# Kernel optimization log

Measured on AMD Instinct MI355X. Metric: run time of the kernel, lower is better.

## Reference

```python
import jax, jax.numpy as jnp
import numpy as np

V = 32000; D = 1024; L = 2; H = 16; KVH = 4; HD = D // H; E = 8; FF = 2048; K = 2
B = 2; S = 1024; WINDOW = 4096; THETA = 10000.0; EPS = 1e-6


def setup_inputs() -> dict:
    key = jax.random.key(0)
    ks = jax.random.split(key, 12)
    std = 0.02
    return {
        'tokens': jax.random.randint(ks[0], (B, S), 0, V),
        'tok_emb': jax.random.normal(ks[1], (V, D), jnp.float32),  # nn.Embedding default N(0,1)
        'norm1_w': jnp.ones((L, D), jnp.float32),
        'norm2_w': jnp.ones((L, D), jnp.float32),
        'wq': jax.random.normal(ks[2], (L, D, D), jnp.float32) * std,
        'wk': jax.random.normal(ks[3], (L, KVH * HD, D), jnp.float32) * std,
        'wv': jax.random.normal(ks[4], (L, KVH * HD, D), jnp.float32) * std,
        'wo': jax.random.normal(ks[5], (L, D, D), jnp.float32) * std,
        'router_w': jax.random.normal(ks[6], (L, E, D), jnp.float32) * (std / np.sqrt(D)),
        'w1': jax.random.normal(ks[7], (L, E, FF, D), jnp.float32) * std,
        'w2': jax.random.normal(ks[8], (L, E, FF, D), jnp.float32) * std,
        'w3': jax.random.normal(ks[9], (L, E, D, FF), jnp.float32) * std,
        'normf_w': jnp.ones((D,), jnp.float32),
        'head_w': jax.random.normal(ks[10], (V, D), jnp.float32) * std,
    }


def rmsnorm(x, w):
    # F.normalize(x, dim=-1, eps) * w * sqrt(d)
    n = jnp.linalg.norm(x, axis=-1, keepdims=True)
    return x / jnp.maximum(n, EPS) * w * np.float32(np.sqrt(x.shape[-1]))


def rope(x, cos, sin):
    # x: (b, s, h, hd); pairs are interleaved (even, odd) per view_as_complex
    x2 = x.reshape(x.shape[:-1] + (-1, 2))
    x0, x1 = x2[..., 0], x2[..., 1]
    o0 = x0 * cos - x1 * sin
    o1 = x0 * sin + x1 * cos
    return jnp.stack([o0, o1], axis=-1).reshape(x.shape)


def attention(x, wq, wk, wv, wo, cos, sin):
    b, s, _ = x.shape
    q = (x @ wq.T).reshape(b, s, H, HD)
    k = (x @ wk.T).reshape(b, s, KVH, HD)
    v = (x @ wv.T).reshape(b, s, KVH, HD)
    q = rope(q, cos, sin)
    k = rope(k, cos, sin)
    g = H // KVH
    k = jnp.repeat(k, g, axis=2)
    v = jnp.repeat(v, g, axis=2)
    scores = jnp.einsum('bqhd,bkhd->bhqk', q, k) / np.float32(np.sqrt(HD))
    i = jnp.arange(s)[:, None]; j = jnp.arange(s)[None, :]
    allow = (j <= i) & (i - j < WINDOW)  # causal + sliding window
    scores = jnp.where(allow, scores, -jnp.inf)
    attn = jax.nn.softmax(scores, axis=-1)
    out = jnp.einsum('bhqk,bkhd->bqhd', attn, v).reshape(b, s, D)
    return out @ wo.T


def moe(x, router_w, w1, w2, w3):
    b, s, d = x.shape
    logits = jnp.einsum('bsd,ed->bse', x, router_w)
    probs = jax.nn.softmax(logits, axis=-1)
    _, idx = jax.lax.top_k(probs, K)                      # (b, s, K)
    mask = jax.nn.one_hot(idx, E, dtype=x.dtype).sum(-2)  # (b, s, E) binary
    xt = x.reshape(-1, d)           # (T, d)
    mt = mask.reshape(-1, E)        # (T, E)
    # Dense masked dispatch: every expert computed on all tokens, combine masks to zero
    u = jnp.einsum('td,efd->etf', xt, w1)
    g = jax.nn.silu(u) * jnp.einsum('td,efd->etf', xt, w2)
    y = jnp.einsum('etf,edf->etd', g, w3)
    out = jnp.einsum('etd,te->td', y, mt).reshape(b, s, d)  # unweighted combine (per source)
    # aux losses
    z_loss = jnp.mean(jax.scipy.special.logsumexp(logits, axis=-1)) ** 2
    load = probs.sum(axis=0)  # (s, E), matching probs.sum(dim=0) in source
    load_loss = (jnp.std(load, ddof=1) / jnp.mean(load)) ** 2
    aux = 0.001 * z_loss + 0.001 * load_loss
    return out, aux


def _rope_tables(dtype):
    freqs = 1.0 / (THETA ** (np.arange(0, HD, 2, dtype=np.float32) / HD))
    ang = np.arange(S, dtype=np.float32)[:, None] * freqs[None, :]
    cos = jnp.asarray(np.cos(ang), dtype)[None, :, None, :]
    sin = jnp.asarray(np.sin(ang), dtype)[None, :, None, :]
    return cos, sin


def reference(tokens, tok_emb, norm1_w, norm2_w, wq, wk, wv, wo, router_w, w1, w2, w3, normf_w, head_w):
    x = tok_emb[tokens]  # (B, S, D)
    cos, sin = _rope_tables(x.dtype)
    attn_scale = np.float32(1.0 / np.sqrt(2.0 * L))
    aux_total = jnp.zeros((), x.dtype)
    for l in range(L):
        x = x + attn_scale * attention(rmsnorm(x, norm1_w[l]), wq[l], wk[l], wv[l], wo[l], cos, sin)
        mo, aux = moe(rmsnorm(x, norm2_w[l]), router_w[l], w1[l], w2[l], w3[l])
        x = x + mo
        aux_total = aux_total + aux
    logits = rmsnorm(x, normf_w) @ head_w.T
    return logits, aux_total
```

## Files before the change

### kernel.cpp

```cpp
#include <hip/hip_runtime.h>
#include <math.h>

#define DEV __device__ __forceinline__

using v8s = __attribute__((ext_vector_type(8))) short;
using v4f = __attribute__((ext_vector_type(4))) float;

DEV short f2bf(float f) {
    unsigned u = __float_as_uint(f);
    unsigned r = (u + 0x7fffu + ((u >> 16) & 1u)) >> 16;
    return (short)(unsigned short)r;
}
DEV float bf2f(short s) {
    return __uint_as_float(((unsigned)(unsigned short)s) << 16);
}

DEV void gload16(const short* g, short* l) {
    __builtin_amdgcn_global_load_lds((const __attribute__((address_space(1))) void*)g,
                                     (__attribute__((address_space(3))) void*)l,
                                     16, 0, 0);
}

DEV float block_sum256(float v, float* red) {
    __syncthreads();
#pragma unroll
    for (int o = 32; o >= 1; o >>= 1) v += __shfl_down(v, o, 64);
    if ((threadIdx.x & 63) == 0) red[threadIdx.x >> 6] = v;
    __syncthreads();
    return red[0] + red[1] + red[2] + red[3];
}
DEV float block_max256(float v, float* red) {
    __syncthreads();
#pragma unroll
    for (int o = 32; o >= 1; o >>= 1) v = fmaxf(v, __shfl_down(v, o, 64));
    if ((threadIdx.x & 63) == 0) red[threadIdx.x >> 6] = v;
    __syncthreads();
    return fmaxf(fmaxf(red[0], red[1]), fmaxf(red[2], red[3]));
}


__global__ __launch_bounds__(256) void conv_tile(const float* __restrict__ src,
                                                 short* __restrict__ hi, short* __restrict__ lo,
                                                 long nGroups, int Kg, long chunkRows, long chunkPanelStride) {
    const long panelElems = 128L * Kg * 8;
    for (long idx = (long)blockIdx.x * 256 + threadIdx.x; idx < nGroups; idx += (long)gridDim.x * 256) {
        long rrow = idx / Kg; int g = (int)(idx - rrow * Kg);
        int kblk = g >> 2, kg = g & 3;
        long c = rrow / chunkRows; int ri = (int)(rrow - c * chunkRows);
        long panel = c * chunkPanelStride + (ri >> 7);
        int row = ri & 127;
        long dst = panel * panelElems + (long)kblk * 4096 + kg * 1024 + row * 8;
        const float4 f0 = ((const float4*)src)[idx * 2];
        const float4 f1 = ((const float4*)src)[idx * 2 + 1];
        short h0 = f2bf(f0.x), h1 = f2bf(f0.y), h2 = f2bf(f0.z), h3 = f2bf(f0.w);
        short h4 = f2bf(f1.x), h5 = f2bf(f1.y), h6 = f2bf(f1.z), h7 = f2bf(f1.w);
        *(ushort4*)(hi + dst)     = make_ushort4((unsigned short)h0, (unsigned short)h1,
                                                 (unsigned short)h2, (unsigned short)h3);
        *(ushort4*)(hi + dst + 4) = make_ushort4((unsigned short)h4, (unsigned short)h5,
                                                 (unsigned short)h6, (unsigned short)h7);
        if (lo) {
            short l0 = f2bf(f0.x - bf2f(h0)), l1 = f2bf(f0.y - bf2f(h1));
            short l2 = f2bf(f0.z - bf2f(h2)), l3 = f2bf(f0.w - bf2f(h3));
            short l4 = f2bf(f1.x - bf2f(h4)), l5 = f2bf(f1.y - bf2f(h5));
            short l6 = f2bf(f1.z - bf2f(h6)), l7 = f2bf(f1.w - bf2f(h7));
            *(ushort4*)(lo + dst)     = make_ushort4((unsigned short)l0, (unsigned short)l1,
                                                     (unsigned short)l2, (unsigned short)l3);
            *(ushort4*)(lo + dst + 4) = make_ushort4((unsigned short)l4, (unsigned short)l5,
                                                     (unsigned short)l6, (unsigned short)l7);
        }
    }
}

struct GemmP {
    const short* Ah; const short* Al;
    const short* Bh; const short* Bl;
    float* C; short* Ch; short* Cl;
    const int* cnt; const int* prefix; const int* ltok; const int* lrow;
    long strideAz, strideBz, strideCz;
    int M, N, K, lda, ldc;
    float alpha;
    int outMode;
    int gqaB;
    int attnC;
    int grouped;
    int causalSkip;
    int causalK;
    int ntiles, S, G;
};

template<bool SPLIT>
__global__ __launch_bounds__(256) void gemm_bt(GemmP p) {
    const int lid = blockIdx.x;
    const int xcd = lid & 7, sI = lid >> 3;
    const int gi = xcd + 8 * (sI / p.S);
    if (gi >= p.G) return;
    const int mt = sI % p.S;
    const int nt = gi % p.ntiles;
    const int z  = gi / p.ntiles;
    if (p.causalSkip && nt > mt) return;

    const int tid = threadIdx.x;

    int Mz = p.M;
    const int* ltokz = nullptr; const int* lrowz = nullptr; int pz = 0;
    if (p.grouped) {
        Mz = p.cnt[z]; pz = p.prefix[z];
        ltokz = p.ltok + z * 2048; lrowz = p.lrow + z * 2048;
    }
    if (mt * 128 >= Mz) return;

    long aOff = (long)z * p.strideAz;
    long bOff, cOff;
    if (p.gqaB) { int b = z >> 4, h = z & 15; bOff = (long)(b * 4 + (h >> 2)) * p.strideBz; }
    else bOff = (long)z * p.strideBz;
    if (p.attnC) { int b = z >> 4, h = z & 15; cOff = (long)b * 1048576 + h * 64; }
    else cOff = (long)z * p.strideCz;

    extern __shared__ char smem[];
    short* Ahs = (short*)smem;
    short* Bhs = Ahs + 4096;
    short* Als = Bhs + 4096;
    short* Bls = Als + 4096;

    const int lane = tid & 63, w = tid >> 6;
    const int lr = lane & 15, lg = lane >> 4;
    const int wr = w >> 1, wc = w & 1;

    v4f acc[4][4];
#pragma unroll
    for (int i = 0; i < 4; ++i)
#pragma unroll
        for (int j = 0; j < 4; ++j) { acc[i][j][0] = 0.f; acc[i][j][1] = 0.f; acc[i][j][2] = 0.f; acc[i][j][3] = 0.f; }

    const int r = tid & 127;
    const int kgA = tid >> 7;
    int am = mt * 128 + r; if (am >= Mz) am = Mz - 1;
    long arowoff;
    if (p.grouped == 1)      arowoff = (long)ltokz[am] * p.lda;
    else if (p.grouped == 2) arowoff = (long)(pz + am) * p.lda;
    else                     arowoff = aOff + (long)am * p.lda;
    const short* aH = p.Ah + arowoff + kgA * 16;
    const short* aL = SPLIT ? p.Al + arowoff + kgA * 16 : nullptr;
    short* sA0 = Ahs + (kgA * 256 + r) * 8;
    short* sA1 = sA0 + 1024;
    short* sA0l = Als + (kgA * 256 + r) * 8;
    short* sA1l = sA0l + 1024;

    const short* bks  = p.Bh + bOff + (long)nt * 128 * p.K + (long)w * 1024 + lane * 8;
    const short* bksL = SPLIT ? p.Bl + bOff + (long)nt * 128 * p.K + (long)w * 1024 + lane * 8 : nullptr;
    short* dB  = Bhs + w * 1024;
    short* dBl = Bls + w * 1024;

    const int kEnd = p.causalK ? min(p.K, (mt + 1) * 128) : p.K;

    for (int k0 = 0; k0 < kEnd; k0 += 32) {
        const long kb = (long)k0 * 128;
        uint4 a0 = *(const uint4*)(aH + k0);
        uint4 a1 = *(const uint4*)(aH + k0 + 8);
        uint4 a0l, a1l;
        if (SPLIT) { a0l = *(const uint4*)(aL + k0); a1l = *(const uint4*)(aL + k0 + 8); }
        __syncthreads();
        gload16(bks + kb,       dB);
        gload16(bks + kb + 512, dB + 512);
        if (SPLIT) {
            gload16(bksL + kb,       dBl);
            gload16(bksL + kb + 512, dBl + 512);
        }
        *(uint4*)sA0 = a0; *(uint4*)sA1 = a1;
        if (SPLIT) { *(uint4*)sA0l = a0l; *(uint4*)sA1l = a1l; }
        __syncthreads();
        const int abase = lg * 1024 + (wr * 64 + lr) * 8;
        const int bbase = lg * 1024 + (wc * 64 + lr) * 8;
        v8s ah[4], bh[4];
#pragma unroll
        for (int i = 0; i < 4; ++i) {
            ah[i] = *(const v8s*)(Ahs + abase + i * 128);
            bh[i] = *(const v8s*)(Bhs + bbase + i * 128);
        }
        if constexpr (SPLIT) {
            v8s al[4], bl[4];
#pragma unroll
            for (int i = 0; i < 4; ++i) {
                al[i] = *(const v8s*)(Als + abase + i * 128);
                bl[i] = *(const v8s*)(Bls + bbase + i * 128);
            }
#pragma unroll
            for (int mi = 0; mi < 4; ++mi)
#pragma unroll
                for (int nj = 0; nj < 4; ++nj) {
                    acc[mi][nj] = __builtin_amdgcn_mfma_f32_16x16x32_bf16(ah[mi], bh[nj], acc[mi][nj], 0, 0, 0);
                    acc[mi][nj] = __builtin_amdgcn_mfma_f32_16x16x32_bf16(al[mi], bh[nj], acc[mi][nj], 0, 0, 0);
                    acc[mi][nj] = __builtin_amdgcn_mfma_f32_16x16x32_bf16(ah[mi], bl[nj], acc[mi][nj], 0, 0, 0);
                }
        } else {
#pragma unroll
            for (int mi = 0; mi < 4; ++mi)
#pragma unroll
                for (int nj = 0; nj < 4; ++nj)
                    acc[mi][nj] = __builtin_amdgcn_mfma_f32_16x16x32_bf16(ah[mi], bh[nj], acc[mi][nj], 0, 0, 0);
        }
    }

#pragma unroll
    for (int mi = 0; mi < 4; ++mi) {
        const int mrow = mt * 128 + wr * 64 + mi * 16 + lg * 4;
#pragma unroll
        for (int nj = 0; nj < 4; ++nj) {
            const int ncol = nt * 128 + wc * 64 + nj * 16 + lr;
            if (ncol < p.N) {
#pragma unroll
                for (int rr = 0; rr < 4; ++rr) {
                    const int m = mrow + rr;
                    if (m < Mz) {
                        float v = acc[mi][nj][rr] * p.alpha;
                        long crow;
                        if (p.grouped == 1) crow = pz + m;
                        else if (p.grouped == 2) crow = lrowz[m];
                        else crow = m;
                        long co = cOff + crow * (long)p.ldc + ncol;
                        if (p.outMode == 0) p.C[co] = v;
                        else if (p.outMode == 1) p.C[co] += v;
                        else {
                            short hi = f2bf(v);
                            p.Ch[co] = hi;
                            p.Cl[co] = f2bf(v - bf2f(hi));
                        }
                    }
                }
            }
        }
    }
}

__global__ __launch_bounds__(256) void embed_kernel(const int* toks, const float* emb, float* X) {
    const int t = blockIdx.x;
    const int tok = toks[t];
    const float4* s = (const float4*)(emb + (size_t)tok * 1024);
    float4* d = (float4*)(X + (size_t)t * 1024);
    d[threadIdx.x] = s[threadIdx.x];
}

__global__ __launch_bounds__(256) void rmsnorm_split(const float* X, const float* w, short* oh, short* ol) {
    __shared__ float red[4];
    const long t = blockIdx.x;
    const float* r = X + t * 1024;
    float ss = 0.f;
    for (int j = threadIdx.x; j < 1024; j += 256) { float f = r[j]; ss += f * f; }
    ss = block_sum256(ss, red);
    const float sc = 32.f / fmaxf(sqrtf(ss), 1e-6f);
    for (int j = threadIdx.x; j < 1024; j += 256) {
        float f = r[j] * sc * w[j];
        short hi = f2bf(f);
        oh[t * 1024 + j] = hi;
        ol[t * 1024 + j] = f2bf(f - bf2f(hi));
    }
}

struct RopeF { float f[32]; };

__global__ __launch_bounds__(256) void rope_q_kernel(const float* QKV, short* OH, short* OL, RopeF rf) {
    const int idx = blockIdx.x * 256 + threadIdx.x;
    const int pp = idx & 31, h = (idx >> 5) & 15, s = (idx >> 9) & 1023, b = idx >> 19;
    const float* src = QKV + ((size_t)(b * 1024 + s)) * 1536 + h * 64 + 2 * pp;
    const float x0 = src[0], x1 = src[1];
    const float ang = (float)s * rf.f[pp];
    float sn, cs; sincosf(ang, &sn, &cs);
    const float o0 = x0 * cs - x1 * sn, o1 = x0 * sn + x1 * cs;
    const size_t o = ((size_t)((b * 16 + h) * 1024 + s)) * 64 + 2 * pp;
    short h0 = f2bf(o0); OH[o] = h0; OL[o] = f2bf(o0 - bf2f(h0));
    short h1 = f2bf(o1); OH[o + 1] = h1; OL[o + 1] = f2bf(o1 - bf2f(h1));
}

__global__ __launch_bounds__(256) void rope_k_kernel(const float* QKV, short* KH, short* KL, RopeF rf) {
    const int idx = blockIdx.x * 256 + threadIdx.x;
    const int pp = idx & 31, kv = (idx >> 5) & 3, s = (idx >> 7) & 1023, b = idx >> 17;
    const float* src = QKV + ((size_t)(b * 1024 + s)) * 1536 + 1024 + kv * 64 + 2 * pp;
    const float x0 = src[0], x1 = src[1];
    const float ang = (float)s * rf.f[pp];
    float sn, cs; sincosf(ang, &sn, &cs);
    const float o0 = x0 * cs - x1 * sn, o1 = x0 * sn + x1 * cs;
    const int z = b * 4 + kv, d = 2 * pp;
    const long off = (long)z * 65536 + (long)(s >> 7) * 8192
                   + ((long)(d >> 5) << 12) + ((long)((d >> 3) & 3) << 10)
                   + ((long)(s & 127) << 3) + (d & 7);
    short h0 = f2bf(o0); KH[off] = h0; KL[off] = f2bf(o0 - bf2f(h0));
    short h1 = f2bf(o1); KH[off + 1] = h1; KL[off + 1] = f2bf(o1 - bf2f(h1));
}

__global__ __launch_bounds__(256) void transpose_v_kernel(const float* QKV, short* VH, short* VL) {
    const int idx = blockIdx.x * 256 + threadIdx.x;
    const int d = idx & 63, kv = (idx >> 6) & 3, s = (idx >> 8) & 1023, b = idx >> 18;
    const float f = QKV[((size_t)(b * 1024 + s)) * 1536 + 1280 + kv * 64 + d];
    const int z = b * 4 + kv;
    const long off = (long)z * 131072 + ((long)(s >> 5) << 12) + ((long)((s >> 3) & 3) << 10)
                   + ((long)d << 3) + (s & 7);
    short hi = f2bf(f);
    VH[off] = hi; VL[off] = f2bf(f - bf2f(hi));
    VH[off + 512] = 0; VL[off + 512] = 0;
}

__global__ __launch_bounds__(256) void attn_softmax(float* SC) {
    const long row = blockIdx.x;
    const int i = (int)(row & 1023);
    float* r = SC + row * 1024;
    __shared__ float buf[1024];
    __shared__ float red[4];
    const int n = i + 1;
    for (int j = threadIdx.x; j < 1024; j += 256) buf[j] = r[j];
    __syncthreads();
    float m = -INFINITY;
    for (int j = threadIdx.x; j < n; j += 256) m = fmaxf(m, buf[j]);
    m = block_max256(m, red);
    float s = 0.f;
    for (int j = threadIdx.x; j < n; j += 256) { float e = expf(buf[j] - m); buf[j] = e; s += e; }
    s = block_sum256(s, red);
    const float inv = 1.f / s;
    short* rh = (short*)r;
    short* rl = rh + 1024;
    __syncthreads();
    for (int j = threadIdx.x; j < 1024; j += 256) {
        float pv = (j < n) ? buf[j] * inv : 0.f;
        short hi = f2bf(pv);
        rh[j] = hi;
        rl[j] = f2bf(pv - bf2f(hi));
    }
}

__global__ __launch_bounds__(256) void router_kernel(const float* X, const float* wn, const float* rw,
                                                     float* probs, float* lse, int* cnt, int* ltok, int* lrow) {
    __shared__ float xs[1024];
    __shared__ float red[4];
    __shared__ float lg[8];
    const int t = blockIdx.x;
    const float* r = X + (size_t)t * 1024;
    for (int j = threadIdx.x; j < 1024; j += 256) xs[j] = r[j];
    __syncthreads();
    float ss = 0.f;
    for (int j = threadIdx.x; j < 1024; j += 256) ss += xs[j] * xs[j];
    ss = block_sum256(ss, red);
    const float sc = 32.f / fmaxf(sqrtf(ss), 1e-6f);
    float acc[8] = {0, 0, 0, 0, 0, 0, 0, 0};
    for (int j = threadIdx.x; j < 1024; j += 256) {
        const float xv = xs[j] * wn[j];
#pragma unroll
        for (int e = 0; e < 8; ++e) acc[e] += xv * rw[e * 1024 + j];
    }
#pragma unroll
    for (int e = 0; e < 8; ++e) {
        float s = block_sum256(acc[e], red);
        if (threadIdx.x == 0) lg[e] = s * sc;
    }
    __syncthreads();
    if (threadIdx.x == 0) {
        float m = lg[0];
        for (int e = 1; e < 8; ++e) m = fmaxf(m, lg[e]);
        float ex[8], se = 0.f;
        for (int e = 0; e < 8; ++e) { ex[e] = expf(lg[e] - m); se += ex[e]; }
        const float inv = 1.f / se;
        float pr[8];
        for (int e = 0; e < 8; ++e) { pr[e] = ex[e] * inv; probs[(size_t)t * 8 + e] = pr[e]; }
        lse[t] = m + logf(se);
        int i1 = 0;
        for (int e = 1; e < 8; ++e) if (pr[e] > pr[i1]) i1 = e;
        int i2 = (i1 == 0) ? 1 : 0;
        for (int e = 0; e < 8; ++e) if (e != i1 && pr[e] > pr[i2]) i2 = e;
        int s1 = atomicAdd(&cnt[i1], 1); ltok[i1 * 2048 + s1] = t; lrow[i1 * 2048 + s1] = 2 * t;
        int s2 = atomicAdd(&cnt[i2], 1); ltok[i2 * 2048 + s2] = t; lrow[i2 * 2048 + s2] = 2 * t + 1;
    }
}

__global__ void prefix_kernel(const int* cnt, int* pref) {
    if (threadIdx.x == 0 && blockIdx.x == 0) {
        int a = 0;
        for (int e = 0; e < 8; ++e) { pref[e] = a; a += cnt[e]; }
    }
}

__global__ __launch_bounds__(256) void silu_mul(const float* U, short* HH, short* HL) {
    const long i4 = (long)blockIdx.x * 256 + threadIdx.x;
    const int f4 = (int)(i4 & 511), row = (int)(i4 >> 9);
    const float4 u = *(const float4*)(U + ((long)row << 12) + (f4 << 2));
    const float4 g = *(const float4*)(U + ((long)row << 12) + 2048 + (f4 << 2));
    float h[4];
    h[0] = (u.x / (1.f + expf(-u.x))) * g.x;
    h[1] = (u.y / (1.f + expf(-u.y))) * g.y;
    h[2] = (u.z / (1.f + expf(-u.z))) * g.z;
    h[3] = (u.w / (1.f + expf(-u.w))) * g.w;
    const long o = (long)row * 2048 + (f4 << 2);
    short h0 = f2bf(h[0]), h1 = f2bf(h[1]), h2 = f2bf(h[2]), h3 = f2bf(h[3]);
    *(ushort4*)(HH + o) = make_ushort4((unsigned short)h0, (unsigned short)h1,
                                       (unsigned short)h2, (unsigned short)h3);
    short l0 = f2bf(h[0] - bf2f(h0)), l1 = f2bf(h[1] - bf2f(h1));
    short l2 = f2bf(h[2] - bf2f(h2)), l3 = f2bf(h[3] - bf2f(h3));
    *(ushort4*)(HL + o) = make_ushort4((unsigned short)l0, (unsigned short)l1,
                                       (unsigned short)l2, (unsigned short)l3);
}

__global__ __launch_bounds__(256) void combine_kernel(float* X, const float* Y) {
    const int i4 = blockIdx.x * 256 + threadIdx.x;
    const int t = i4 >> 8, d4 = i4 & 255;
    float4 x = ((float4*)X)[i4];
    const float4 a = ((const float4*)Y)[(size_t)(2 * t) * 256 + d4];
    const float4 b = ((const float4*)Y)[(size_t)(2 * t + 1) * 256 + d4];
    x.x += a.x + b.x; x.y += a.y + b.y; x.z += a.z + b.z; x.w += a.w + b.w;
    ((float4*)X)[i4] = x;
}

__global__ __launch_bounds__(256) void aux_kernel(const float* probs, const float* lse, float* auxb, int layer) {
    __shared__ float red[4];
    float sl = 0.f;
    for (int t = threadIdx.x; t < 2048; t += 256) sl += lse[t];
    sl = block_sum256(sl, red);
    float s1 = 0.f, s2 = 0.f;
    for (int i = threadIdx.x; i < 8192; i += 256) {
        const float l = probs[i] + probs[8192 + i];
        s1 += l; s2 += l * l;
    }
    s1 = block_sum256(s1, red);
    s2 = block_sum256(s2, red);
    if (threadIdx.x == 0) {
        const float ml = sl / 2048.f;
        const float mean = s1 / 8192.f;
        const float var = fmaxf((s2 - s1 * s1 / 8192.f) / 8191.f, 0.f);
        auxb[layer] = 0.001f * (ml * ml + var / (mean * mean));
    }
}

__global__ void finalize_aux(const float* auxb, float* out) {
    if (threadIdx.x == 0 && blockIdx.x == 0)
        out[(size_t)2 * 1024 * 32000] = auxb[0] + auxb[1];
}

static void run_gemm(hipStream_t s, bool split, GemmP& p, int ntiles, int mtiles, int zdim) {
    p.ntiles = ntiles; p.S = mtiles;
    p.G = ntiles * zdim;
    int Gp = (p.G + 7) & ~7;
    long nb = (long)Gp * mtiles;
    dim3 g((unsigned)nb, 1, 1), b(256);
    if (split) gemm_bt<true><<<g, b, 32768, s>>>(p);
    else       gemm_bt<false><<<g, b, 16384, s>>>(p);
}

static void run_tile(hipStream_t s, const float* src, short* hi, short* lo,
                     long rows, int K, long chunkRows, long chunkPanelStride) {
    long groups = rows * (K / 8);
    long nb = (groups + 255) / 256; if (nb > 2048) nb = 2048;
    conv_tile<<<(unsigned)nb, 256, 0, s>>>(src, hi, lo, groups, K / 8, chunkRows, chunkPanelStride);
}

extern "C" void kernel_launch(void* const* d_in, const int* in_sizes, int n_in,
                              void* d_out, int out_size, void* d_ws, size_t ws_size,
                              hipStream_t stream) {
    (void)in_sizes; (void)n_in; (void)out_size; (void)ws_size;
    const int*   tokens = (const int*)d_in[0];
    const float* tok_emb = (const float*)d_in[1];
    const float* norm1 = (const float*)d_in[2];
    const float* norm2 = (const float*)d_in[3];
    const float* wq = (const float*)d_in[4];
    const float* wk = (const float*)d_in[5];
    const float* wv = (const float*)d_in[6];
    const float* wo = (const float*)d_in[7];
    const float* rw = (const float*)d_in[8];
    const float* w1 = (const float*)d_in[9];
    const float* w2 = (const float*)d_in[10];
    const float* w3 = (const float*)d_in[11];
    const float* normf = (const float*)d_in[12];
    const float* headw = (const float*)d_in[13];
    float* out = (float*)d_out;

    char* w = (char*)d_ws;
    const size_t MB = 1024ull * 1024ull;
    float* X    = (float*)(w + 0);
    short* XNH  = (short*)(w + 8 * MB);
    short* XNL  = (short*)(w + 12 * MB);
    short* QRH  = (short*)(w + 16 * MB);
    short* QRL  = (short*)(w + 20 * MB);
    short* AOH  = QRH;
    short* AOL  = QRL;
    short* KRH  = (short*)(w + 24 * MB);
    short* KRL  = (short*)(w + 25 * MB);
    short* VTH  = (short*)(w + 26 * MB);
    short* VTL  = (short*)(w + 28 * MB);
    float* QKV  = (float*)(w + 32 * MB);
    float* SC   = (float*)(w + 32 * MB);
    float* U    = (float*)(w + 32 * MB);
    short* HH   = (short*)(w + 96 * MB);
    short* HL   = (short*)(w + 112 * MB);
    float* Y    = (float*)(w + 128 * MB);
    float* PROBS= (float*)(w + 160 * MB);
    float* LSE  = (float*)(w + 160 * MB + 65536);
    int*   CNT  = (int*)  (w + 160 * MB + 73728);
    int*   PREF = (int*)  (w + 160 * MB + 73856);
    int*   LTOK = (int*)  (w + 160 * MB + 74240);
    int*   LROW = (int*)  (w + 160 * MB + 74240 + 65536);
    float* AUXB = (float*)(w + 160 * MB + 74240 + 131072);
    short* WQKVH = (short*)(w + 162 * MB);
    short* WQKVL = (short*)(w + 168 * MB);
    short* WOH   = (short*)(w + 174 * MB);
    short* WOL   = (short*)(w + 178 * MB);
    short* W12H  = (short*)(w + 182 * MB);
    short* W12L  = (short*)(w + 246 * MB);
    short* W3H   = (short*)(w + 310 * MB);
    short* W3L   = (short*)(w + 342 * MB);
    short* HDH   = (short*)(w + 374 * MB);

    RopeF rf;
    for (int i = 0; i < 32; ++i) {
        float t = (float)pow(10000.0, (double)(2 * i) / 64.0);
        rf.f[i] = 1.0f / t;
    }

    for (int l = 0; l < 2; ++l) {
        long qo = (long)l * 1572864;
        run_tile(stream, wq + (long)l * 1048576, WQKVH + qo,           WQKVL + qo,           1024, 1024, 1024, 8);
        run_tile(stream, wk + (long)l * 262144,  WQKVH + qo + 1048576, WQKVL + qo + 1048576, 256, 1024, 256, 2);
        run_tile(stream, wv + (long)l * 262144,  WQKVH + qo + 1310720, WQKVL + qo + 1310720, 256, 1024, 256, 2);
    }
    run_tile(stream, wo, WOH, WOL, 2048, 1024, 2048, 16);
    run_tile(stream, headw, HDH, nullptr, 32000, 1024, 32000, 250);

    embed_kernel<<<2048, 256, 0, stream>>>(tokens, tok_emb, X);

    for (int l = 0; l < 2; ++l) {
        const bool msp = (l == 0);
        run_tile(stream, w1 + (long)l * 16777216, W12H,           msp ? W12L : nullptr,           16384, 1024, 2048, 32);
        run_tile(stream, w2 + (long)l * 16777216, W12H + 2097152, msp ? W12L + 2097152 : nullptr, 16384, 1024, 2048, 32);
        run_tile(stream, w3 + (long)l * 16777216, W3H,            msp ? W3L : nullptr,            8192, 2048, 8192, 64);

        rmsnorm_split<<<2048, 256, 0, stream>>>(X, norm1 + l * 1024, XNH, XNL);

        { GemmP p = {}; p.Ah = XNH; p.Al = XNL; p.Bh = WQKVH + (long)l * 1572864; p.Bl = WQKVL + (long)l * 1572864;
          p.C = QKV; p.M = 2048; p.N = 1536; p.K = 1024; p.lda = 1024; p.ldc = 1536; p.alpha = 1.f;
          run_gemm(stream, true, p, 12, 16, 1); }

        rope_q_kernel<<<4096, 256, 0, stream>>>(QKV, QRH, QRL, rf);
        rope_k_kernel<<<1024, 256, 0, stream>>>(QKV, KRH, KRL, rf);
        transpose_v_kernel<<<2048, 256, 0, stream>>>(QKV, VTH, VTL);

        { GemmP p = {}; p.Ah = QRH; p.Al = QRL; p.Bh = KRH; p.Bl = KRL; p.C = SC;
          p.M = 1024; p.N = 1024; p.K = 64; p.lda = 64; p.ldc = 1024;
          p.strideAz = 65536; p.strideBz = 65536; p.strideCz = 1048576;
          p.alpha = 0.125f; p.gqaB = 1; p.causalSkip = 1;
          run_gemm(stream, true, p, 8, 8, 32); }

        attn_softmax<<<32768, 256, 0, stream>>>(SC);

        { GemmP p = {}; p.Ah = (short*)SC; p.Al = (short*)SC + 1024; p.Bh = VTH; p.Bl = VTL; p.Ch = AOH; p.Cl = AOL;
          p.M = 1024; p.N = 64; p.K = 1024; p.lda = 2048; p.ldc = 1024;
          p.strideAz = 2097152; p.strideBz = 131072;
          p.alpha = 1.f; p.gqaB = 1; p.attnC = 1; p.causalK = 1; p.outMode = 2;
          run_gemm(stream, true, p, 1, 8, 32); }

        { GemmP p = {}; p.Ah = AOH; p.Al = AOL; p.Bh = WOH + (long)l * 1048576; p.Bl = WOL + (long)l * 1048576; p.C = X;
          p.M = 2048; p.N = 1024; p.K = 1024; p.lda = 1024; p.ldc = 1024;
          p.alpha = 0.5f; p.outMode = 1;
          run_gemm(stream, true, p, 8, 16, 1); }

        rmsnorm_split<<<2048, 256, 0, stream>>>(X, norm2 + l * 1024, XNH, XNL);
        hipMemsetAsync(CNT, 0, 8 * sizeof(int), stream);
        router_kernel<<<2048, 256, 0, stream>>>(X, norm2 + l * 1024, rw + (size_t)l * 8 * 1024,
                                                PROBS, LSE, CNT, LTOK, LROW);
        prefix_kernel<<<1, 64, 0, stream>>>(CNT, PREF);

        { GemmP p = {}; p.Ah = XNH; p.Al = XNL; p.Bh = W12H; p.Bl = W12L; p.C = U;
          p.M = 2048; p.N = 4096; p.K = 1024; p.lda = 1024; p.ldc = 4096;
          p.strideBz = 4194304; p.alpha = 1.f; p.grouped = 1;
          p.cnt = CNT; p.prefix = PREF; p.ltok = LTOK; p.lrow = LROW;
          run_gemm(stream, msp, p, 32, 16, 8); }
        silu_mul<<<8192, 256, 0, stream>>>(U, HH, HL);
        { GemmP p = {}; p.Ah = HH; p.Al = HL; p.Bh = W3H; p.Bl = W3L; p.C = Y;
          p.M = 2048; p.N = 1024; p.K = 2048; p.lda = 2048; p.ldc = 1024;
          p.strideBz = 2097152; p.alpha = 1.f; p.grouped = 2;
          p.cnt = CNT; p.prefix = PREF; p.ltok = LTOK; p.lrow = LROW;
          run_gemm(stream, msp, p, 8, 16, 8); }
        combine_kernel<<<2048, 256, 0, stream>>>(X, Y);
        aux_kernel<<<1, 256, 0, stream>>>(PROBS, LSE, AUXB, l);
    }

    rmsnorm_split<<<2048, 256, 0, stream>>>(X, normf, XNH, XNL);
    { GemmP p = {}; p.Ah = XNH; p.Bh = HDH; p.C = out;
      p.M = 2048; p.N = 32000; p.K = 1024; p.lda = 1024; p.ldc = 32000; p.alpha = 1.f;
      run_gemm(stream, false, p, 250, 16, 1); }
    finalize_aux<<<1, 1, 0, stream>>>(AUXB, out);
}
```

Before: 2.310 ms.

## Pre-tile GEMM A operands so A loads use direct global-to-LDS copies

Producers of GEMM A operands (rmsnorm, rope_q, silu_mul, the attention output epilogue) now write the same 128-row panel layout used for B. The GEMM can then stream A through global_load_lds instead of register loads followed by LDS stores. MoE tokens are gathered into per-expert padded panels by a new gather kernel, and the head weight conversion is moved later so it can share buffer space with the W12 low half. The cost is an extra gather pass, padded expert segments, and scattered per-element stores in the rope and attention epilogues.

Result: slower. 2.375 ms (+2.8%).

```diff
diff --git a/kernel.cpp b/kernel.cpp
--- a/kernel.cpp
+++ b/kernel.cpp
@@ -36,6 +36,10 @@
     if ((threadIdx.x & 63) == 0) red[threadIdx.x >> 6] = v;
     __syncthreads();
     return fmaxf(fmaxf(red[0], red[1]), fmaxf(red[2], red[3]));
+}
+
+DEV long tile_goff(int row, int g) {
+    return ((long)(g >> 2) << 12) + ((long)(g & 3) << 10) + ((long)(row & 127) << 3);
 }
 
 
@@ -45,11 +49,9 @@
     const long panelElems = 128L * Kg * 8;
     for (long idx = (long)blockIdx.x * 256 + threadIdx.x; idx < nGroups; idx += (long)gridDim.x * 256) {
         long rrow = idx / Kg; int g = (int)(idx - rrow * Kg);
-        int kblk = g >> 2, kg = g & 3;
         long c = rrow / chunkRows; int ri = (int)(rrow - c * chunkRows);
         long panel = c * chunkPanelStride + (ri >> 7);
-        int row = ri & 127;
-        long dst = panel * panelElems + (long)kblk * 4096 + kg * 1024 + row * 8;
+        long dst = panel * panelElems + ((long)(g >> 2) << 12) + ((long)(g & 3) << 10) + ((long)(ri & 127) << 3);
         const float4 f0 = ((const float4*)src)[idx * 2];
         const float4 f1 = ((const float4*)src)[idx * 2 + 1];
         short h0 = f2bf(f0.x), h1 = f2bf(f0.y), h2 = f2bf(f0.z), h3 = f2bf(f0.w);
@@ -75,20 +77,21 @@
     const short* Ah; const short* Al;
     const short* Bh; const short* Bl;
     float* C; short* Ch; short* Cl;
-    const int* cnt; const int* prefix; const int* ltok; const int* lrow;
-    long strideAz, strideBz, strideCz;
+    const int* cnt; const int* ppd; const int* lrow;
+    long aPanelsZ;
+    long strideAz;
+    long strideBz, strideCz;
     int M, N, K, lda, ldc;
     float alpha;
     int outMode;
     int gqaB;
-    int attnC;
     int grouped;
     int causalSkip;
     int causalK;
     int ntiles, S, G;
 };
 
-template<bool SPLIT>
+template<bool SPLIT, bool AREG>
 __global__ __launch_bounds__(256) void gemm_bt(GemmP p) {
     const int lid = blockIdx.x;
     const int xcd = lid & 7, sI = lid >> 3;
@@ -101,20 +104,12 @@
 
     const int tid = threadIdx.x;
 
-    int Mz = p.M;
-    const int* ltokz = nullptr; const int* lrowz = nullptr; int pz = 0;
-    if (p.grouped) {
-        Mz = p.cnt[z]; pz = p.prefix[z];
-        ltokz = p.ltok + z * 2048; lrowz = p.lrow + z * 2048;
-    }
+    int Mz = p.grouped ? p.cnt[z] : p.M;
     if (mt * 128 >= Mz) return;
 
-    long aOff = (long)z * p.strideAz;
-    long bOff, cOff;
+    long bOff;
     if (p.gqaB) { int b = z >> 4, h = z & 15; bOff = (long)(b * 4 + (h >> 2)) * p.strideBz; }
     else bOff = (long)z * p.strideBz;
-    if (p.attnC) { int b = z >> 4, h = z & 15; cOff = (long)b * 1048576 + h * 64; }
-    else cOff = (long)z * p.strideCz;
 
     extern __shared__ char smem[];
     short* Ahs = (short*)smem;
@@ -132,33 +127,42 @@
 #pragma unroll
         for (int j = 0; j < 4; ++j) { acc[i][j][0] = 0.f; acc[i][j][1] = 0.f; acc[i][j][2] = 0.f; acc[i][j][3] = 0.f; }
 
-    const int r = tid & 127;
-    const int kgA = tid >> 7;
-    int am = mt * 128 + r; if (am >= Mz) am = Mz - 1;
-    long arowoff;
-    if (p.grouped == 1)      arowoff = (long)ltokz[am] * p.lda;
-    else if (p.grouped == 2) arowoff = (long)(pz + am) * p.lda;
-    else                     arowoff = aOff + (long)am * p.lda;
-    const short* aH = p.Ah + arowoff + kgA * 16;
-    const short* aL = SPLIT ? p.Al + arowoff + kgA * 16 : nullptr;
-    short* sA0 = Ahs + (kgA * 256 + r) * 8;
-    short* sA1 = sA0 + 1024;
-    short* sA0l = Als + (kgA * 256 + r) * 8;
-    short* sA1l = sA0l + 1024;
-
     const short* bks  = p.Bh + bOff + (long)nt * 128 * p.K + (long)w * 1024 + lane * 8;
     const short* bksL = SPLIT ? p.Bl + bOff + (long)nt * 128 * p.K + (long)w * 1024 + lane * 8 : nullptr;
     short* dB  = Bhs + w * 1024;
     short* dBl = Bls + w * 1024;
 
+    const short *aks = nullptr, *aksL = nullptr;
+    short *dA = nullptr, *dAl = nullptr;
+    const short *aH = nullptr, *aL = nullptr;
+    short *sA0 = nullptr, *sA1 = nullptr, *sA0l = nullptr, *sA1l = nullptr;
+    if constexpr (AREG) {
+        const int r = tid & 127;
+        const int kgA = tid >> 7;
+        int am = mt * 128 + r; if (am >= Mz) am = Mz - 1;
+        long arowoff = (long)z * p.strideAz + (long)am * p.lda;
+        aH = p.Ah + arowoff + kgA * 16;
+        aL = SPLIT ? p.Al + arowoff + kgA * 16 : nullptr;
+        sA0 = Ahs + (kgA * 256 + r) * 8; sA1 = sA0 + 1024;
+        sA0l = Als + (kgA * 256 + r) * 8; sA1l = sA0l + 1024;
+    } else {
+        long aPanel = (p.grouped ? (long)(p.ppd[z] >> 7) : (long)z * p.aPanelsZ) + mt;
+        aks  = p.Ah + aPanel * 128L * p.K + (long)w * 1024 + lane * 8;
+        aksL = SPLIT ? p.Al + aPanel * 128L * p.K + (long)w * 1024 + lane * 8 : nullptr;
+        dA  = Ahs + w * 1024;
+        dAl = Als + w * 1024;
+    }
+
     const int kEnd = p.causalK ? min(p.K, (mt + 1) * 128) : p.K;
 
     for (int k0 = 0; k0 < kEnd; k0 += 32) {
         const long kb = (long)k0 * 128;
-        uint4 a0 = *(const uint4*)(aH + k0);
-        uint4 a1 = *(const uint4*)(aH + k0 + 8);
-        uint4 a0l, a1l;
-        if (SPLIT) { a0l = *(const uint4*)(aL + k0); a1l = *(const uint4*)(aL + k0 + 8); }
+        uint4 a0, a1, a0l, a1l;
+        if constexpr (AREG) {
+            a0 = *(const uint4*)(aH + k0);
+            a1 = *(const uint4*)(aH + k0 + 8);
+            if (SPLIT) { a0l = *(const uint4*)(aL + k0); a1l = *(const uint4*)(aL + k0 + 8); }
+        }
         __syncthreads();
         gload16(bks + kb,       dB);
         gload16(bks + kb + 512, dB + 512);
@@ -166,8 +170,17 @@
             gload16(bksL + kb,       dBl);
             gload16(bksL + kb + 512, dBl + 512);
         }
-        *(uint4*)sA0 = a0; *(uint4*)sA1 = a1;
-        if (SPLIT) { *(uint4*)sA0l = a0l; *(uint4*)sA1l = a1l; }
+        if constexpr (AREG) {
+            *(uint4*)sA0 = a0; *(uint4*)sA1 = a1;
+            if (SPLIT) { *(uint4*)sA0l = a0l; *(uint4*)sA1l = a1l; }
+        } else {
+            gload16(aks + kb,       dA);
+            gload16(aks + kb + 512, dA + 512);
+            if (SPLIT) {
+                gload16(aksL + kb,       dAl);
+                gload16(aksL + kb + 512, dAl + 512);
+            }
+        }
         __syncthreads();
         const int abase = lg * 1024 + (wr * 64 + lr) * 8;
         const int bbase = lg * 1024 + (wc * 64 + lr) * 8;
@@ -213,17 +226,22 @@
                     const int m = mrow + rr;
                     if (m < Mz) {
                         float v = acc[mi][nj][rr] * p.alpha;
-                        long crow;
-                        if (p.grouped == 1) crow = pz + m;
-                        else if (p.grouped == 2) crow = lrowz[m];
-                        else crow = m;
-                        long co = cOff + crow * (long)p.ldc + ncol;
-                        if (p.outMode == 0) p.C[co] = v;
-                        else if (p.outMode == 1) p.C[co] += v;
-                        else {
+                        if (p.outMode == 3) {
+                            int b = z >> 4, h = z & 15;
+                            int grow = b * 1024 + m, col = h * 64 + ncol;
+                            long dst = ((long)(grow >> 7)) * 131072 + ((long)(col >> 5) << 12)
+                                     + ((long)((col >> 3) & 3) << 10) + ((long)(grow & 127) << 3) + (col & 7);
                             short hi = f2bf(v);
-                            p.Ch[co] = hi;
-                            p.Cl[co] = f2bf(v - bf2f(hi));
+                            p.Ch[dst] = hi;
+                            p.Cl[dst] = f2bf(v - bf2f(hi));
+                        } else {
+                            long crow;
+                            if (p.grouped == 1)      crow = p.ppd[z] + m;
+                            else if (p.grouped == 2) crow = p.lrow[z * 2048 + m];
+                            else                     crow = m;
+                            long co = (long)z * p.strideCz + crow * (long)p.ldc + ncol;
+                            if (p.outMode == 0) p.C[co] = v;
+                            else                p.C[co] += v;
                         }
                     }
                 }
@@ -248,11 +266,19 @@
     for (int j = threadIdx.x; j < 1024; j += 256) { float f = r[j]; ss += f * f; }
     ss = block_sum256(ss, red);
     const float sc = 32.f / fmaxf(sqrtf(ss), 1e-6f);
-    for (int j = threadIdx.x; j < 1024; j += 256) {
-        float f = r[j] * sc * w[j];
-        short hi = f2bf(f);
-        oh[t * 1024 + j] = hi;
-        ol[t * 1024 + j] = f2bf(f - bf2f(hi));
+    if (threadIdx.x < 128) {
+        const int g = threadIdx.x, f = g * 8;
+        float v[8];
+#pragma unroll
+        for (int j = 0; j < 8; ++j) v[j] = r[f + j] * sc * w[f + j];
+        long dst = (t >> 7) * 131072 + ((long)(g >> 2) << 12) + ((long)(g & 3) << 10) + ((t & 127) << 3);
+        short h[8], lo[8];
+#pragma unroll
+        for (int j = 0; j < 8; ++j) { h[j] = f2bf(v[j]); lo[j] = f2bf(v[j] - bf2f(h[j])); }
+        *(ushort4*)(oh + dst)     = make_ushort4((unsigned short)h[0], (unsigned short)h[1], (unsigned short)h[2], (unsigned short)h[3]);
+        *(ushort4*)(oh + dst + 4) = make_ushort4((unsigned short)h[4], (unsigned short)h[5], (unsigned short)h[6], (unsigned short)h[7]);
+        *(ushort4*)(ol + dst)     = make_ushort4((unsigned short)lo[0], (unsigned short)lo[1], (unsigned short)lo[2], (unsigned short)lo[3]);
+        *(ushort4*)(ol + dst + 4) = make_ushort4((unsigned short)lo[4], (unsigned short)lo[5], (unsigned short)lo[6], (unsigned short)lo[7]);
     }
 }
 
@@ -266,9 +292,12 @@
     const float ang = (float)s * rf.f[pp];
     float sn, cs; sincosf(ang, &sn, &cs);
     const float o0 = x0 * cs - x1 * sn, o1 = x0 * sn + x1 * cs;
-    const size_t o = ((size_t)((b * 16 + h) * 1024 + s)) * 64 + 2 * pp;
-    short h0 = f2bf(o0); OH[o] = h0; OL[o] = f2bf(o0 - bf2f(h0));
-    short h1 = f2bf(o1); OH[o + 1] = h1; OL[o + 1] = f2bf(o1 - bf2f(h1));
+    const int z = b * 16 + h, d = 2 * pp;
+    const long off = (long)z * 65536 + (long)(s >> 7) * 8192
+                   + ((long)(d >> 5) << 12) + ((long)((d >> 3) & 3) << 10)
+                   + ((long)(s & 127) << 3) + (d & 7);
+    short h0 = f2bf(o0); OH[off] = h0; OL[off] = f2bf(o0 - bf2f(h0));
+    short h1 = f2bf(o1); OH[off + 1] = h1; OL[off + 1] = f2bf(o1 - bf2f(h1));
 }
 
 __global__ __launch_bounds__(256) void rope_k_kernel(const float* QKV, short* KH, short* KL, RopeF rf) {
@@ -369,31 +398,51 @@
     }
 }
 
-__global__ void prefix_kernel(const int* cnt, int* pref) {
+__global__ void prefix_kernel(const int* cnt, int* ppd) {
     if (threadIdx.x == 0 && blockIdx.x == 0) {
         int a = 0;
-        for (int e = 0; e < 8; ++e) { pref[e] = a; a += cnt[e]; }
-    }
+        for (int e = 0; e < 8; ++e) { ppd[e] = a; a += ((cnt[e] + 127) >> 7) << 7; }
+    }
+}
+
+__global__ __launch_bounds__(256) void gather_kernel(const short* XNH, const short* XNL,
+                                                     const int* cnt, const int* ppd, const int* ltok,
+                                                     short* GXNH, short* GXNL) {
+    const int e = blockIdx.y, i = blockIdx.x;
+    if (i >= cnt[e]) return;
+    const int t = ltok[e * 2048 + i];
+    const int pd = ppd[e] + i;
+    const int plane = threadIdx.x >> 7, g = threadIdx.x & 127;
+    const long goff = ((long)(g >> 2) << 12) + ((long)(g & 3) << 10);
+    const long src = (long)(t >> 7) * 131072 + goff + ((t & 127) << 3);
+    const long dst = (long)(pd >> 7) * 131072 + goff + ((pd & 127) << 3);
+    const short* S = plane ? XNL : XNH;
+    short* D = plane ? GXNL : GXNH;
+    *(uint4*)(D + dst) = *(const uint4*)(S + src);
 }
 
 __global__ __launch_bounds__(256) void silu_mul(const float* U, short* HH, short* HL) {
-    const long i4 = (long)blockIdx.x * 256 + threadIdx.x;
-    const int f4 = (int)(i4 & 511), row = (int)(i4 >> 9);
-    const float4 u = *(const float4*)(U + ((long)row << 12) + (f4 << 2));
-    const float4 g = *(const float4*)(U + ((long)row << 12) + 2048 + (f4 << 2));
-    float h[4];
-    h[0] = (u.x / (1.f + expf(-u.x))) * g.x;
-    h[1] = (u.y / (1.f + expf(-u.y))) * g.y;
-    h[2] = (u.z / (1.f + expf(-u.z))) * g.z;
-    h[3] = (u.w / (1.f + expf(-u.w))) * g.w;
-    const long o = (long)row * 2048 + (f4 << 2);
-    short h0 = f2bf(h[0]), h1 = f2bf(h[1]), h2 = f2bf(h[2]), h3 = f2bf(h[3]);
-    *(ushort4*)(HH + o) = make_ushort4((unsigned short)h0, (unsigned short)h1,
-                                       (unsigned short)h2, (unsigned short)h3);
-    short l0 = f2bf(h[0] - bf2f(h0)), l1 = f2bf(h[1] - bf2f(h1));
-    short l2 = f2bf(h[2] - bf2f(h2)), l3 = f2bf(h[3] - bf2f(h3));
-    *(ushort4*)(HL + o) = make_ushort4((unsigned short)l0, (unsigned short)l1,
-                                       (unsigned short)l2, (unsigned short)l3);
+    const int row = blockIdx.x, g = threadIdx.x;
+    const float* ur = U + (long)row * 4096 + g * 8;
+    const float4 u0 = *(const float4*)ur, u1 = *(const float4*)(ur + 4);
+    const float4 g0 = *(const float4*)(ur + 2048), g1 = *(const float4*)(ur + 2052);
+    float h[8];
+    h[0] = (u0.x / (1.f + expf(-u0.x))) * g0.x;
+    h[1] = (u0.y / (1.f + expf(-u0.y))) * g0.y;
+    h[2] = (u0.z / (1.f + expf(-u0.z))) * g0.z;
+    h[3] = (u0.w / (1.f + expf(-u0.w))) * g0.w;
+    h[4] = (u1.x / (1.f + expf(-u1.x))) * g1.x;
+    h[5] = (u1.y / (1.f + expf(-u1.y))) * g1.y;
+    h[6] = (u1.z / (1.f + expf(-u1.z))) * g1.z;
+    h[7] = (u1.w / (1.f + expf(-u1.w))) * g1.w;
+    const long dst = (long)(row >> 7) * 262144 + ((long)(g >> 2) << 12) + ((long)(g & 3) << 10) + ((row & 127) << 3);
+    short hh[8], ll[8];
+#pragma unroll
+    for (int j = 0; j < 8; ++j) { hh[j] = f2bf(h[j]); ll[j] = f2bf(h[j] - bf2f(hh[j])); }
+    *(ushort4*)(HH + dst)     = make_ushort4((unsigned short)hh[0], (unsigned short)hh[1], (unsigned short)hh[2], (unsigned short)hh[3]);
+    *(ushort4*)(HH + dst + 4) = make_ushort4((unsigned short)hh[4], (unsigned short)hh[5], (unsigned short)hh[6], (unsigned short)hh[7]);
+    *(ushort4*)(HL + dst)     = make_ushort4((unsigned short)ll[0], (unsigned short)ll[1], (unsigned short)ll[2], (unsigned short)ll[3]);
+    *(ushort4*)(HL + dst + 4) = make_ushort4((unsigned short)ll[4], (unsigned short)ll[5], (unsigned short)ll[6], (unsigned short)ll[7]);
 }
 
 __global__ __launch_bounds__(256) void combine_kernel(float* X, const float* Y) {
@@ -431,14 +480,19 @@
         out[(size_t)2 * 1024 * 32000] = auxb[0] + auxb[1];
 }
 
-static void run_gemm(hipStream_t s, bool split, GemmP& p, int ntiles, int mtiles, int zdim) {
+static void run_gemm(hipStream_t s, bool split, bool areg, GemmP& p, int ntiles, int mtiles, int zdim) {
     p.ntiles = ntiles; p.S = mtiles;
     p.G = ntiles * zdim;
     int Gp = (p.G + 7) & ~7;
     long nb = (long)Gp * mtiles;
     dim3 g((unsigned)nb, 1, 1), b(256);
-    if (split) gemm_bt<true><<<g, b, 32768, s>>>(p);
-    else       gemm_bt<false><<<g, b, 16384, s>>>(p);
+    if (split) {
+        if (areg) gemm_bt<true, true><<<g, b, 32768, s>>>(p);
+        else      gemm_bt<true, false><<<g, b, 32768, s>>>(p);
+    } else {
+        if (areg) gemm_bt<false, true><<<g, b, 16384, s>>>(p);
+        else      gemm_bt<false, false><<<g, b, 16384, s>>>(p);
+    }
 }
 
 static void run_tile(hipStream_t s, const float* src, short* hi, short* lo,
@@ -484,25 +538,27 @@
     float* QKV  = (float*)(w + 32 * MB);
     float* SC   = (float*)(w + 32 * MB);
     float* U    = (float*)(w + 32 * MB);
-    short* HH   = (short*)(w + 96 * MB);
-    short* HL   = (short*)(w + 112 * MB);
-    float* Y    = (float*)(w + 128 * MB);
-    float* PROBS= (float*)(w + 160 * MB);
-    float* LSE  = (float*)(w + 160 * MB + 65536);
-    int*   CNT  = (int*)  (w + 160 * MB + 73728);
-    int*   PREF = (int*)  (w + 160 * MB + 73856);
-    int*   LTOK = (int*)  (w + 160 * MB + 74240);
-    int*   LROW = (int*)  (w + 160 * MB + 74240 + 65536);
-    float* AUXB = (float*)(w + 160 * MB + 74240 + 131072);
-    short* WQKVH = (short*)(w + 162 * MB);
-    short* WQKVL = (short*)(w + 168 * MB);
-    short* WOH   = (short*)(w + 174 * MB);
-    short* WOL   = (short*)(w + 178 * MB);
-    short* W12H  = (short*)(w + 182 * MB);
-    short* W12L  = (short*)(w + 246 * MB);
-    short* W3H   = (short*)(w + 310 * MB);
-    short* W3L   = (short*)(w + 342 * MB);
-    short* HDH   = (short*)(w + 374 * MB);
+    short* HH   = (short*)(w + 112 * MB);
+    short* HL   = (short*)(w + 132 * MB);
+    float* Y    = (float*)(w + 152 * MB);
+    short* GXNH = (short*)(w + 168 * MB);
+    short* GXNL = (short*)(w + 178 * MB);
+    float* PROBS= (float*)(w + 188 * MB);
+    float* LSE  = (float*)(w + 188 * MB + 65536);
+    int*   CNT  = (int*)  (w + 188 * MB + 73728);
+    int*   PPD  = (int*)  (w + 188 * MB + 73856);
+    int*   LTOK = (int*)  (w + 188 * MB + 74240);
+    int*   LROW = (int*)  (w + 188 * MB + 74240 + 65536);
+    float* AUXB = (float*)(w + 188 * MB + 74240 + 131072);
+    short* WQKVH = (short*)(w + 190 * MB);
+    short* WQKVL = (short*)(w + 196 * MB);
+    short* WOH   = (short*)(w + 202 * MB);
+    short* WOL   = (short*)(w + 206 * MB);
+    short* W12H  = (short*)(w + 210 * MB);
+    short* W12L  = (short*)(w + 274 * MB);
+    short* W3H   = (short*)(w + 338 * MB);
+    short* W3L   = (short*)(w + 370 * MB);
+    short* HDH   = (short*)(w + 274 * MB);
 
     RopeF rf;
     for (int i = 0; i < 32; ++i) {
@@ -517,7 +573,6 @@
         run_tile(stream, wv + (long)l * 262144,  WQKVH + qo + 1310720, WQKVL + qo + 1310720, 256, 1024, 256, 2);
     }
     run_tile(stream, wo, WOH, WOL, 2048, 1024, 2048, 16);
-    run_tile(stream, headw, HDH, nullptr, 32000, 1024, 32000, 250);
 
     embed_kernel<<<2048, 256, 0, stream>>>(tokens, tok_emb, X);
 
@@ -530,56 +585,60 @@
         rmsnorm_split<<<2048, 256, 0, stream>>>(X, norm1 + l * 1024, XNH, XNL);
 
         { GemmP p = {}; p.Ah = XNH; p.Al = XNL; p.Bh = WQKVH + (long)l * 1572864; p.Bl = WQKVL + (long)l * 1572864;
-          p.C = QKV; p.M = 2048; p.N = 1536; p.K = 1024; p.lda = 1024; p.ldc = 1536; p.alpha = 1.f;
-          run_gemm(stream, true, p, 12, 16, 1); }
+          p.C = QKV; p.M = 2048; p.N = 1536; p.K = 1024; p.aPanelsZ = 16; p.ldc = 1536; p.alpha = 1.f;
+          run_gemm(stream, true, false, p, 12, 16, 1); }
 
         rope_q_kernel<<<4096, 256, 0, stream>>>(QKV, QRH, QRL, rf);
         rope_k_kernel<<<1024, 256, 0, stream>>>(QKV, KRH, KRL, rf);
         transpose_v_kernel<<<2048, 256, 0, stream>>>(QKV, VTH, VTL);
 
         { GemmP p = {}; p.Ah = QRH; p.Al = QRL; p.Bh = KRH; p.Bl = KRL; p.C = SC;
-          p.M = 1024; p.N = 1024; p.K = 64; p.lda = 64; p.ldc = 1024;
-          p.strideAz = 65536; p.strideBz = 65536; p.strideCz = 1048576;
+          p.M = 1024; p.N = 1024; p.K = 64; p.aPanelsZ = 8; p.ldc = 1024;
+          p.strideBz = 65536; p.strideCz = 1048576;
           p.alpha = 0.125f; p.gqaB = 1; p.causalSkip = 1;
-          run_gemm(stream, true, p, 8, 8, 32); }
+          run_gemm(stream, true, false, p, 8, 8, 32); }
 
         attn_softmax<<<32768, 256, 0, stream>>>(SC);
 
         { GemmP p = {}; p.Ah = (short*)SC; p.Al = (short*)SC + 1024; p.Bh = VTH; p.Bl = VTL; p.Ch = AOH; p.Cl = AOL;
-          p.M = 1024; p.N = 64; p.K = 1024; p.lda = 2048; p.ldc = 1024;
+          p.M = 1024; p.N = 64; p.K = 1024; p.lda = 2048;
           p.strideAz = 2097152; p.strideBz = 131072;
-          p.alpha = 1.f; p.gqaB = 1; p.attnC = 1; p.causalK = 1; p.outMode = 2;
-          run_gemm(stream, true, p, 1, 8, 32); }
+          p.alpha = 1.f; p.gqaB = 1; p.causalK = 1; p.outMode = 3;
+          run_gemm(stream, true, true, p, 1, 8, 32); }
 
         { GemmP p = {}; p.Ah = AOH; p.Al = AOL; p.Bh = WOH + (long)l * 1048576; p.Bl = WOL + (long)l * 1048576; p.C = X;
-          p.M = 2048; p.N = 1024; p.K = 1024; p.lda = 1024; p.ldc = 1024;
+          p.M = 2048; p.N = 1024; p.K = 1024; p.aPanelsZ = 16; p.ldc = 1024;
           p.alpha = 0.5f; p.outMode = 1;
-          run_gemm(stream, true, p, 8, 16, 1); }
+          run_gemm(stream, true, false, p, 8, 16, 1); }
 
         rmsnorm_split<<<2048, 256, 0, stream>>>(X, norm2 + l * 1024, XNH, XNL);
         hipMemsetAsync(CNT, 0, 8 * sizeof(int), stream);
         router_kernel<<<2048, 256, 0, stream>>>(X, norm2 + l * 1024, rw + (size_t)l * 8 * 1024,
                                                 PROBS, LSE, CNT, LTOK, LROW);
-        prefix_kernel<<<1, 64, 0, stream>>>(CNT, PREF);
-
-        { GemmP p = {}; p.Ah = XNH; p.Al = XNL; p.Bh = W12H; p.Bl = W12L; p.C = U;
-          p.M = 2048; p.N = 4096; p.K = 1024; p.lda = 1024; p.ldc = 4096;
-          p.strideBz = 4194304; p.alpha = 1.f; p.grouped = 1;
-          p.cnt = CNT; p.prefix = PREF; p.ltok = LTOK; p.lrow = LROW;
-          run_gemm(stream, msp, p, 32, 16, 8); }
-        silu_mul<<<8192, 256, 0, stream>>>(U, HH, HL);
+        prefix_kernel<<<1, 64, 0, stream>>>(CNT, PPD);
+        { dim3 gg(2048, 8); gather_kernel<<<gg, 256, 0, stream>>>(XNH, XNL, CNT, PPD, LTOK, GXNH, GXNL); }
+
+        { GemmP p = {}; p.Ah = GXNH; p.Al = GXNL; p.Bh = W12H; p.Bl = W12L; p.C = U;
+          p.M = 2048; p.N = 4096; p.K = 1024; p.ldc = 4096;
+          p.strideBz = 4194304; p.strideCz = 0; p.alpha = 1.f; p.grouped = 1;
+          p.cnt = CNT; p.ppd = PPD; p.lrow = LROW;
+          run_gemm(stream, msp, false, p, 32, 16, 8); }
+        silu_mul<<<5120, 256, 0, stream>>>(U, HH, HL);
         { GemmP p = {}; p.Ah = HH; p.Al = HL; p.Bh = W3H; p.Bl = W3L; p.C = Y;
-          p.M = 2048; p.N = 1024; p.K = 2048; p.lda = 2048; p.ldc = 1024;
-          p.strideBz = 2097152; p.alpha = 1.f; p.grouped = 2;
-          p.cnt = CNT; p.prefix = PREF; p.ltok = LTOK; p.lrow = LROW;
-          run_gemm(stream, msp, p, 8, 16, 8); }
+          p.M = 2048; p.N = 1024; p.K = 2048; p.ldc = 1024;
+          p.strideBz = 2097152; p.strideCz = 0; p.alpha = 1.f; p.grouped = 2;
+          p.cnt = CNT; p.ppd = PPD; p.lrow = LROW;
+          run_gemm(stream, msp, false, p, 8, 16, 8); }
         combine_kernel<<<2048, 256, 0, stream>>>(X, Y);
         aux_kernel<<<1, 256, 0, stream>>>(PROBS, LSE, AUXB, l);
+
+        if (l == 0)
+            run_tile(stream, headw, HDH, nullptr, 32000, 1024, 32000, 250);
     }
 
     rmsnorm_split<<<2048, 256, 0, stream>>>(X, normf, XNH, XNL);
     { GemmP p = {}; p.Ah = XNH; p.Bh = HDH; p.C = out;
-      p.M = 2048; p.N = 32000; p.K = 1024; p.lda = 1024; p.ldc = 32000; p.alpha = 1.f;
-      run_gemm(stream, false, p, 250, 16, 1); }
+      p.M = 2048; p.N = 32000; p.K = 1024; p.aPanelsZ = 16; p.ldc = 32000; p.alpha = 1.f;
+      run_gemm(stream, false, false, p, 250, 16, 1); }
     finalize_aux<<<1, 1, 0, stream>>>(AUXB, out);
 }
```
